# Performance work log

Measured on AMD Instinct MI355X. Metric: run time of the kernel, lower is better.

## Reference

```python
import jax, jax.numpy as jnp
import numpy as np

N, E, H, NH, RBF = 20000, 200000, 128, 8, 64
HD = H // NH
CUT_HI = 5.0


def _ln(t, s, b, eps=1e-6):
    mu = t.mean(-1, keepdims=True)
    var = ((t - mu) ** 2).mean(-1, keepdims=True)
    return (t - mu) * jax.lax.rsqrt(var + eps) * s + b


def _cutoff(w):
    # cosine cutoff, cutoff_lower = 0
    return 0.5 * (jnp.cos(w * (jnp.pi / CUT_HI)) + 1.0) * (w < CUT_HI)


def _xavier(k, fi, fo):
    lim = float(np.sqrt(6.0 / (fi + fo)))
    return jax.random.uniform(k, (fi, fo), minval=-lim, maxval=lim, dtype=jnp.float32)


def setup_inputs() -> dict:
    key = jax.random.key(0)
    ks = jax.random.split(key, 16)
    return {
        "x": jax.random.normal(ks[0], (N, H), jnp.float32),
        "vec": jax.random.normal(ks[1], (N, 3, H), jnp.float32),
        "edge_weight": jax.random.uniform(ks[2], (E, 1), jnp.float32) * 6.0,
        "edge_attr": jax.random.uniform(ks[3], (E, RBF), jnp.float32),
        "edge_vec": jax.random.normal(ks[4], (E, 3), jnp.float32),
        "senders": jax.random.randint(ks[5], (E,), 0, N, jnp.int32),
        "receivers": jax.random.randint(ks[6], (E,), 0, N, jnp.int32),
        "ln_s": jnp.ones((H,), jnp.float32), "ln_b": jnp.zeros((H,), jnp.float32),
        "Wq": _xavier(ks[7], H, H), "bq": jnp.zeros((H,), jnp.float32),
        "Wk": _xavier(ks[8], H, H), "bk": jnp.zeros((H,), jnp.float32),
        "Wv": _xavier(ks[9], H, 3 * H), "bv": jnp.zeros((3 * H,), jnp.float32),
        "Wvec": _xavier(ks[10], H, 3 * H),
        "Wdk": _xavier(ks[11], RBF, H), "bdk": jnp.zeros((H,), jnp.float32),
        "Wdv": _xavier(ks[12], RBF, 3 * H), "bdv": jnp.zeros((3 * H,), jnp.float32),
        "Wo": _xavier(ks[13], H, 3 * H), "bo": jnp.zeros((3 * H,), jnp.float32),
        "qln_s": jnp.ones((HD,), jnp.float32), "qln_b": jnp.zeros((HD,), jnp.float32),
        "kln_s": jnp.ones((HD,), jnp.float32), "kln_b": jnp.zeros((HD,), jnp.float32),
    }


def reference(x, vec, edge_weight, edge_attr, edge_vec, senders, receivers,
              ln_s, ln_b, Wq, bq, Wk, bk, Wv, bv, Wvec, Wdk, bdk, Wdv, bdv,
              Wo, bo, qln_s, qln_b, kln_s, kln_b):
    act = jax.nn.silu
    n = x.shape[0]
    xn = _ln(x, ln_s, ln_b)                                    # [N,H]
    q = _ln((xn @ Wq + bq).reshape(n, NH, HD), qln_s, qln_b)   # [N,h,d]
    k = _ln((xn @ Wk + bk).reshape(n, NH, HD), kln_s, kln_b)   # [N,h,d]
    v = (xn @ Wv + bv).reshape(n, NH, 3 * HD)                  # [N,h,3d]
    vp = vec @ Wvec                                            # [N,3,3H]
    vec1, vec2, vec3 = jnp.split(vp, 3, axis=-1)               # [N,3,H] each
    vec_dot = (vec1 * vec2).sum(axis=1)                        # [N,H]
    vec_h = vec.reshape(n, 3, NH, HD)                          # [N,3,h,d]
    dk = act(edge_attr @ Wdk + bdk).reshape(-1, NH, HD)        # [E,h,d]
    dv = act(edge_attr @ Wdv + bdv).reshape(-1, NH, 3 * HD)    # [E,h,3d]
    # message
    attn = (q[receivers] * k[senders] * dk).sum(axis=-1)       # [E,h]
    attn = act(attn) * _cutoff(edge_weight)                    # [E,h]
    v_j = v[senders] * dv                                      # [E,h,3d]
    xm, m1, m2 = jnp.split(v_j, 3, axis=2)                     # [E,h,d]
    xm = xm * attn[:, :, None]                                 # [E,h,d]
    vec_m = vec_h[senders] * m1[:, None] + m2[:, None] * edge_vec[:, :, None, None]  # [E,3,h,d]
    # aggregate
    x_agg = jax.ops.segment_sum(xm, receivers, num_segments=n).reshape(n, H)
    vec_agg = jax.ops.segment_sum(vec_m, receivers, num_segments=n).reshape(n, 3, H)
    o1, o2, o3 = jnp.split(x_agg @ Wo + bo, 3, axis=1)         # [N,H] each
    dvec = vec3 * o1[:, None] + vec_agg                        # [N,3,H]
    dx = vec_dot * o2 + o3                                     # [N,H]
    return (dx, dvec)
```

## Files before the change

kernel.cpp:

```cpp
#include <hip/hip_runtime.h>
#include <stdint.h>

#define NN 20000
#define NE 200000

typedef __attribute__((ext_vector_type(8))) short bf16x8;
typedef __attribute__((ext_vector_type(4))) float f32x4;

__device__ __forceinline__ float bf2f(uint32_t u) {
  union { uint32_t i; float f; } v; v.i = u << 16; return v.f;
}
__device__ __forceinline__ uint16_t f2bf(float f) {
  union { float f; uint32_t i; } v; v.f = f;
  return (uint16_t)((v.i + 0x7fffu + ((v.i >> 16) & 1u)) >> 16);
}
__device__ __forceinline__ float siluf(float x) { return x / (1.f + __expf(-x)); }


__global__ void k_transpose_cast(const float* __restrict__ src, uint16_t* __restrict__ dst,
                                 int K, int C) {
  int idx = blockIdx.x * 256 + threadIdx.x;
  if (idx >= K * C) return;
  int c = idx / K, k = idx - c * K;
  dst[idx] = f2bf(src[(size_t)k * C + c]);
}

__global__ void k_bias_concat(const float* __restrict__ bq, const float* __restrict__ bk,
                              const float* __restrict__ bv, const float* __restrict__ bdk,
                              const float* __restrict__ bdv, float* __restrict__ Bqkv,
                              float* __restrict__ Bdkv) {
  int t = blockIdx.x * 256 + threadIdx.x;
  if (t < 640) Bqkv[t] = (t < 128) ? bq[t] : ((t < 256) ? bk[t - 128] : bv[t - 256]);
  if (t < 512) Bdkv[t] = (t < 128) ? bdk[t] : bdv[t - 128];
}

__global__ void k_ln_cast(const float* __restrict__ x, const float* __restrict__ s,
                          const float* __restrict__ b, uint16_t* __restrict__ out) {
  int gt = blockIdx.x * 256 + threadIdx.x;
  int node = gt >> 6, lane = gt & 63;
  if (node >= NN) return;
  const float* row = x + (size_t)node * 128;
  float2 v = *(const float2*)&row[lane * 2];
  float sum = v.x + v.y, sq = v.x * v.x + v.y * v.y;
  #pragma unroll
  for (int off = 32; off; off >>= 1) { sum += __shfl_xor(sum, off); sq += __shfl_xor(sq, off); }
  float mu = sum * (1.f / 128.f);
  float var = sq * (1.f / 128.f) - mu * mu;
  float rs = rsqrtf(var + 1e-6f);
  float o0 = (v.x - mu) * rs * s[lane * 2] + b[lane * 2];
  float o1 = (v.y - mu) * rs * s[lane * 2 + 1] + b[lane * 2 + 1];
  ((uint32_t*)out)[(size_t)node * 64 + lane] = (uint32_t)f2bf(o0) | ((uint32_t)f2bf(o1) << 16);
}

__global__ void k_cast_bf16(const float* __restrict__ src, uint16_t* __restrict__ dst, int npairs) {
  int i = blockIdx.x * 256 + threadIdx.x;
  if (i >= npairs) return;
  float2 v = ((const float2*)src)[i];
  ((uint32_t*)dst)[i] = (uint32_t)f2bf(v.x) | ((uint32_t)f2bf(v.y) << 16);
}

__global__ void k_hist(const int* __restrict__ rcv, int* __restrict__ deg) {
  int e = blockIdx.x * 256 + threadIdx.x;
  if (e < NE) atomicAdd(&deg[rcv[e]], 1);
}

__global__ void k_scan1(const int* __restrict__ deg, int* __restrict__ bsum) {
  __shared__ int ws[4];
  int i = blockIdx.x * 256 + threadIdx.x;
  int x = (i < NN) ? deg[i] : 0;
  #pragma unroll
  for (int d = 32; d; d >>= 1) x += __shfl_xor(x, d);
  if ((threadIdx.x & 63) == 0) ws[threadIdx.x >> 6] = x;
  __syncthreads();
  if (threadIdx.x == 0) bsum[blockIdx.x] = ws[0] + ws[1] + ws[2] + ws[3];
}

__global__ void k_scan2(int* __restrict__ bsum, int nb, int* __restrict__ off) {
  int lane = threadIdx.x;
  int carry = 0;
  for (int base = 0; base < nb; base += 64) {
    int i = base + lane;
    int x = (i < nb) ? bsum[i] : 0;
    int v = x;
    #pragma unroll
    for (int d = 1; d < 64; d <<= 1) { int y = __shfl_up(v, d); if (lane >= d) v += y; }
    if (i < nb) bsum[i] = carry + v - x;
    carry += __shfl(v, 63);
  }
  if (lane == 0) off[NN] = carry;
}

__global__ void k_scan3(const int* __restrict__ deg, const int* __restrict__ bsum,
                        int* __restrict__ off, int* __restrict__ cur) {
  __shared__ int ws[4];
  int t = threadIdx.x, lane = t & 63, w = t >> 6;
  int i = blockIdx.x * 256 + t;
  int x = (i < NN) ? deg[i] : 0;
  int v = x;
  #pragma unroll
  for (int d = 1; d < 64; d <<= 1) { int y = __shfl_up(v, d); if (lane >= d) v += y; }
  if (lane == 63) ws[w] = v;
  __syncthreads();
  int wadd = 0;
  for (int j = 0; j < w; j++) wadd += ws[j];
  int excl = bsum[blockIdx.x] + wadd + v - x;
  if (i < NN) { off[i] = excl; cur[i] = excl; }
}

__global__ void k_scatter(const int* __restrict__ rcv, int* __restrict__ cur,
                          int* __restrict__ perm) {
  int e = blockIdx.x * 256 + threadIdx.x;
  if (e >= NE) return;
  int pos = atomicAdd(&cur[rcv[e]], 1);
  perm[pos] = e;
}

__global__ void k_permute(const float* __restrict__ ea, const int* __restrict__ perm,
                          const int* __restrict__ snd, const float* __restrict__ ew,
                          const float* __restrict__ evec, uint16_t* __restrict__ ea_perm,
                          int* __restrict__ sndp, float4* __restrict__ edata) {
  int idx = blockIdx.x * 256 + threadIdx.x;
  if (idx >= NE * 16) return;
  int i = idx >> 4, j = idx & 15;
  int e = perm[i];
  float4 v = *(const float4*)&ea[(size_t)e * 64 + j * 4];
  uint2 o;
  o.x = (uint32_t)f2bf(v.x) | ((uint32_t)f2bf(v.y) << 16);
  o.y = (uint32_t)f2bf(v.z) | ((uint32_t)f2bf(v.w) << 16);
  *(uint2*)&ea_perm[(size_t)i * 64 + j * 4] = o;
  if (j == 0) {
    sndp[i] = snd[e];
    edata[i] = make_float4(evec[e * 3], evec[e * 3 + 1], evec[e * 3 + 2], ew[e]);
  }
}

template <int KTOT, bool OUT_BF16, bool SILU>
__global__ __launch_bounds__(256) void k_gemm(const uint16_t* __restrict__ A,
                                              const uint16_t* __restrict__ BT,
                                              const float* __restrict__ bias,
                                              void* __restrict__ Cout, int M, int Fo) {
  __shared__ __align__(16) uint16_t As[128 * 72];
  __shared__ __align__(16) uint16_t Bs[128 * 72];
  int t = threadIdx.x;
  int l = t & 63;
  int row0 = blockIdx.y * 128, col0 = blockIdx.x * 128;
  int wm = ((t >> 6) >> 1) * 64, wn = ((t >> 6) & 1) * 64;
  f32x4 acc[4][4] = {};
  for (int kt = 0; kt < KTOT; kt += 64) {
    __syncthreads();
    #pragma unroll
    for (int i = 0; i < 4; i++) {
      int c = i * 256 + t;
      int row = c >> 3, ko = (c & 7) * 8;
      uint4 av = make_uint4(0u, 0u, 0u, 0u);
      int gr = row0 + row;
      if (gr < M) av = *(const uint4*)&A[(size_t)gr * KTOT + kt + ko];
      *(uint4*)&As[row * 72 + ko] = av;
      uint4 bw = *(const uint4*)&BT[(size_t)(col0 + row) * KTOT + kt + ko];
      *(uint4*)&Bs[row * 72 + ko] = bw;
    }
    __syncthreads();
    #pragma unroll
    for (int kk = 0; kk < 64; kk += 32) {
      bf16x8 af[4], bfr[4];
      #pragma unroll
      for (int mf = 0; mf < 4; mf++)
        af[mf] = *(const bf16x8*)&As[(wm + mf * 16 + (l & 15)) * 72 + (l >> 4) * 8 + kk];
      #pragma unroll
      for (int nf = 0; nf < 4; nf++)
        bfr[nf] = *(const bf16x8*)&Bs[(wn + nf * 16 + (l & 15)) * 72 + (l >> 4) * 8 + kk];
      #pragma unroll
      for (int mf = 0; mf < 4; mf++)
        #pragma unroll
        for (int nf = 0; nf < 4; nf++)
          acc[mf][nf] = __builtin_amdgcn_mfma_f32_16x16x32_bf16(af[mf], bfr[nf], acc[mf][nf], 0, 0, 0);
    }
  }
  float* Cf = (float*)Cout;
  uint16_t* Cb = (uint16_t*)Cout;
  #pragma unroll
  for (int mf = 0; mf < 4; mf++) {
    #pragma unroll
    for (int r = 0; r < 4; r++) {
      int grow = row0 + wm + mf * 16 + (l >> 4) * 4 + r;
      if (grow >= M) continue;
      #pragma unroll
      for (int nf = 0; nf < 4; nf++) {
        int gcol = col0 + wn + nf * 16 + (l & 15);
        float v = acc[mf][nf][r];
        if (bias) v += bias[gcol];
        if (SILU) v = siluf(v);
        if (OUT_BF16) Cb[(size_t)grow * Fo + gcol] = f2bf(v);
        else          Cf[(size_t)grow * Fo + gcol] = v;
      }
    }
  }
}

__global__ __launch_bounds__(256) void k_gemm_dkv(const uint16_t* __restrict__ Aperm,
                                                  const int* __restrict__ pbeg,
                                                  const int* __restrict__ pend,
                                                  const uint16_t* __restrict__ BT,
                                                  const float* __restrict__ bias,
                                                  uint16_t* __restrict__ Cout, int Mcap) {
  int e0 = pbeg[0];
  int M = pend[0] - e0;
  if (M > Mcap) M = Mcap;
  int row0 = blockIdx.y * 128, col0 = blockIdx.x * 128;
  if (row0 >= M) return;
  const uint16_t* A = Aperm + (size_t)e0 * 64;
  __shared__ __align__(16) uint16_t As[128 * 72];
  __shared__ __align__(16) uint16_t Bs[128 * 72];
  int t = threadIdx.x;
  int l = t & 63;
  int wm = ((t >> 6) >> 1) * 64, wn = ((t >> 6) & 1) * 64;
  f32x4 acc[4][4] = {};
  {
    #pragma unroll
    for (int i = 0; i < 4; i++) {
      int c = i * 256 + t;
      int row = c >> 3, ko = (c & 7) * 8;
      uint4 av = make_uint4(0u, 0u, 0u, 0u);
      if (row0 + row < M) av = *(const uint4*)&A[(size_t)(row0 + row) * 64 + ko];
      *(uint4*)&As[row * 72 + ko] = av;
      uint4 bw = *(const uint4*)&BT[(size_t)(col0 + row) * 64 + ko];
      *(uint4*)&Bs[row * 72 + ko] = bw;
    }
    __syncthreads();
    #pragma unroll
    for (int kk = 0; kk < 64; kk += 32) {
      bf16x8 af[4], bfr[4];
      #pragma unroll
      for (int mf = 0; mf < 4; mf++)
        af[mf] = *(const bf16x8*)&As[(wm + mf * 16 + (l & 15)) * 72 + (l >> 4) * 8 + kk];
      #pragma unroll
      for (int nf = 0; nf < 4; nf++)
        bfr[nf] = *(const bf16x8*)&Bs[(wn + nf * 16 + (l & 15)) * 72 + (l >> 4) * 8 + kk];
      #pragma unroll
      for (int mf = 0; mf < 4; mf++)
        #pragma unroll
        for (int nf = 0; nf < 4; nf++)
          acc[mf][nf] = __builtin_amdgcn_mfma_f32_16x16x32_bf16(af[mf], bfr[nf], acc[mf][nf], 0, 0, 0);
    }
  }
  #pragma unroll
  for (int mf = 0; mf < 4; mf++) {
    #pragma unroll
    for (int r = 0; r < 4; r++) {
      int grow = row0 + wm + mf * 16 + (l >> 4) * 4 + r;
      if (grow >= M) continue;
      #pragma unroll
      for (int nf = 0; nf < 4; nf++) {
        int gcol = col0 + wn + nf * 16 + (l & 15);
        float v = siluf(acc[mf][nf][r] + bias[gcol]);
        Cout[(size_t)grow * 512 + gcol] = f2bf(v);
      }
    }
  }
}

__global__ void k_headln(const uint16_t* __restrict__ qkv, const float* __restrict__ qs,
                         const float* __restrict__ qb, const float* __restrict__ ks,
                         const float* __restrict__ kb, uint16_t* __restrict__ out) {
  int idx = blockIdx.x * 256 + threadIdx.x;
  if (idx >= NN * 16) return;
  int n = idx >> 4, ph = idx & 15, part = ph >> 3, h = ph & 7;
  const uint16_t* src = qkv + (size_t)n * 640 + part * 128 + h * 16;
  float v[16], sum = 0.f;
  #pragma unroll
  for (int i = 0; i < 16; i++) { v[i] = bf2f(src[i]); sum += v[i]; }
  float mu = sum * (1.f / 16.f), var = 0.f;
  #pragma unroll
  for (int i = 0; i < 16; i++) { float d = v[i] - mu; var += d * d; }
  float rs = rsqrtf(var * (1.f / 16.f) + 1e-6f);
  const float* sc = part ? ks : qs;
  const float* bb = part ? kb : qb;
  uint16_t* dst = out + (size_t)n * 256 + part * 128 + h * 16;
  #pragma unroll
  for (int i = 0; i < 16; i++) dst[i] = f2bf((v[i] - mu) * rs * sc[i] + bb[i]);
}

__global__ __launch_bounds__(128) void k_agg(
    const uint16_t* __restrict__ dkdv, const int* __restrict__ off,
    const int* __restrict__ sndp, const float4* __restrict__ edata,
    const uint16_t* __restrict__ qk_b, const uint16_t* __restrict__ qkv_b,
    const uint16_t* __restrict__ vec_b, float* __restrict__ xagg,
    float* __restrict__ vecagg, int n0, int n1, int Mcap) {
  int n = n0 + blockIdx.x;
  if (n >= n1) return;
  int hd = threadIdx.x, h = hd >> 4, d = hd & 15;
  int i0 = off[n], i1 = off[n + 1];
  int ebase = off[n0];
  float q = bf2f(qk_b[(size_t)n * 256 + hd]);
  int vb = h * 48 + d;
  float ax = 0.f, a0 = 0.f, a1 = 0.f, a2 = 0.f;
  for (int i = i0; i < i1; i++) {
    int li = i - ebase;
    if (li >= Mcap) break;
    int s = sndp[i];
    float4 ed = edata[i];
    const uint16_t* row = dkdv + (size_t)li * 512;
    float dk = bf2f(row[hd]);
    float kv = bf2f(qk_b[(size_t)s * 256 + 128 + hd]);
    float t = q * kv * dk;
    t += __shfl_xor(t, 1); t += __shfl_xor(t, 2);
    t += __shfl_xor(t, 4); t += __shfl_xor(t, 8);
    float w = ed.w;
    float cut = (w < 5.f) ? 0.5f * (__cosf(w * 0.628318530717958648f) + 1.f) : 0.f;
    float a = (t / (1.f + __expf(-t))) * cut;
    float dv0 = bf2f(row[128 + vb]), dv1 = bf2f(row[144 + vb]), dv2 = bf2f(row[160 + vb]);
    const uint16_t* vsp = qkv_b + (size_t)s * 640 + 256 + vb;
    float m1 = bf2f(vsp[16]) * dv1;
    float m2 = bf2f(vsp[32]) * dv2;
    ax += bf2f(vsp[0]) * dv0 * a;
    const uint16_t* vv = vec_b + (size_t)s * 384;
    a0 += bf2f(vv[hd]) * m1 + m2 * ed.x;
    a1 += bf2f(vv[128 + hd]) * m1 + m2 * ed.y;
    a2 += bf2f(vv[256 + hd]) * m1 + m2 * ed.z;
  }
  xagg[(size_t)n * 128 + hd] = ax;
  vecagg[((size_t)n * 3 + 0) * 128 + hd] = a0;
  vecagg[((size_t)n * 3 + 1) * 128 + hd] = a1;
  vecagg[((size_t)n * 3 + 2) * 128 + hd] = a2;
}

__global__ void k_final(const float* __restrict__ o, const uint16_t* __restrict__ vp,
                        float* __restrict__ dx, float* __restrict__ dvec) {
  int idx = blockIdx.x * 256 + threadIdx.x;
  if (idx >= NN * 128) return;
  int n = idx >> 7, j = idx & 127;
  const float* op = o + (size_t)n * 384;
  float o1 = op[j], o2 = op[128 + j], o3 = op[256 + j];
  const uint16_t* vpn = vp + (size_t)n * 3 * 384;
  float vd = 0.f;
  #pragma unroll
  for (int c = 0; c < 3; c++)
    vd += bf2f(vpn[c * 384 + j]) * bf2f(vpn[c * 384 + 128 + j]);
  dx[idx] = vd * o2 + o3;
  #pragma unroll
  for (int c = 0; c < 3; c++) {
    size_t vi = ((size_t)n * 3 + c) * 128 + j;
    dvec[vi] = bf2f(vpn[c * 384 + 256 + j]) * o1 + dvec[vi];
  }
}

static inline int cdiv_i(long long a, long long b) { return (int)((a + b - 1) / b); }

extern "C" void kernel_launch(void* const* d_in, const int* in_sizes, int n_in,
                              void* d_out, int out_size, void* d_ws, size_t ws_size,
                              hipStream_t stream) {
  const float* x    = (const float*)d_in[0];
  const float* vec  = (const float*)d_in[1];
  const float* ew   = (const float*)d_in[2];
  const float* ea   = (const float*)d_in[3];
  const float* evec = (const float*)d_in[4];
  const int*   snd  = (const int*)d_in[5];
  const int*   rcv  = (const int*)d_in[6];
  const float* ln_s = (const float*)d_in[7];
  const float* ln_b = (const float*)d_in[8];
  const float* Wq = (const float*)d_in[9];   const float* bq = (const float*)d_in[10];
  const float* Wk = (const float*)d_in[11];  const float* bk = (const float*)d_in[12];
  const float* Wv = (const float*)d_in[13];  const float* bv = (const float*)d_in[14];
  const float* Wvec = (const float*)d_in[15];
  const float* Wdk = (const float*)d_in[16]; const float* bdk = (const float*)d_in[17];
  const float* Wdv = (const float*)d_in[18]; const float* bdv = (const float*)d_in[19];
  const float* Wo = (const float*)d_in[20];  const float* bo = (const float*)d_in[21];
  const float* qln_s = (const float*)d_in[22]; const float* qln_b = (const float*)d_in[23];
  const float* kln_s = (const float*)d_in[24]; const float* kln_b = (const float*)d_in[25];
  (void)in_sizes; (void)n_in; (void)out_size;

  uint8_t* p = (uint8_t*)d_ws;
  auto alloc = [&](size_t bytes) -> uint8_t* {
    uint8_t* r = p; p += (bytes + 255) & ~(size_t)255; return r;
  };
  uint16_t* WTqkv = (uint16_t*)alloc(640 * 128 * 2);
  float*    Bqkv  = (float*)alloc(640 * 4);
  uint16_t* WTvec = (uint16_t*)alloc(384 * 128 * 2);
  uint16_t* WTdkv = (uint16_t*)alloc(512 * 64 * 2);
  float*    Bdkv  = (float*)alloc(512 * 4);
  uint16_t* WTo   = (uint16_t*)alloc(384 * 128 * 2);
  int*      deg   = (int*)alloc(NN * 4);
  int*      off   = (int*)alloc((NN + 1) * 4);
  int*      cur   = (int*)alloc(NN * 4);
  int*      bsum  = (int*)alloc(256 * 4);
  int*      perm  = (int*)alloc((size_t)NE * 4);
  int*      sndp  = (int*)alloc((size_t)NE * 4);
  float4*   edata = (float4*)alloc((size_t)NE * 16);
  uint16_t* xn_b  = (uint16_t*)alloc((size_t)NN * 128 * 2);
  uint16_t* qkv_b = (uint16_t*)alloc((size_t)NN * 640 * 2);
  uint16_t* qk_b  = (uint16_t*)alloc((size_t)NN * 256 * 2);
  uint16_t* vec_b = (uint16_t*)alloc((size_t)NN * 3 * 128 * 2);
  uint16_t* vp    = (uint16_t*)alloc((size_t)NN * 3 * 384 * 2);
  uint16_t* ea_perm = (uint16_t*)alloc((size_t)NE * 64 * 2);
  float*    o      = (float*)alloc((size_t)NN * 384 * 4);
  uint16_t* xagg_b = (uint16_t*)alloc((size_t)NN * 128 * 2);
  size_t fixed = (size_t)(p - (uint8_t*)d_ws);

  int nchunk = 1;
  long long CHmax = NE;
  for (nchunk = 1; nchunk <= 64; nchunk++) {
    long long base = (NE + nchunk - 1) / nchunk;
    CHmax = (nchunk == 1) ? (long long)NE : base + base / 4;
    if (fixed + (size_t)CHmax * 1024 + 4096 <= ws_size) break;
  }
  uint16_t* dkdv = (uint16_t*)alloc((size_t)CHmax * 1024);
  int NB = cdiv_i(NN, nchunk);

  float* xagg   = (float*)d_out;
  float* vecagg = (float*)d_out + (size_t)NN * 128;

  k_transpose_cast<<<cdiv_i(128 * 128, 256), 256, 0, stream>>>(Wq, WTqkv, 128, 128);
  k_transpose_cast<<<cdiv_i(128 * 128, 256), 256, 0, stream>>>(Wk, WTqkv + 128 * 128, 128, 128);
  k_transpose_cast<<<cdiv_i(384 * 128, 256), 256, 0, stream>>>(Wv, WTqkv + 256 * 128, 128, 384);
  k_transpose_cast<<<cdiv_i(384 * 128, 256), 256, 0, stream>>>(Wvec, WTvec, 128, 384);
  k_transpose_cast<<<cdiv_i(128 * 64, 256), 256, 0, stream>>>(Wdk, WTdkv, 64, 128);
  k_transpose_cast<<<cdiv_i(384 * 64, 256), 256, 0, stream>>>(Wdv, WTdkv + 128 * 64, 64, 384);
  k_transpose_cast<<<cdiv_i(384 * 128, 256), 256, 0, stream>>>(Wo, WTo, 128, 384);
  k_bias_concat<<<3, 256, 0, stream>>>(bq, bk, bv, bdk, bdv, Bqkv, Bdkv);

  int NSB = cdiv_i(NN, 256);
  hipMemsetAsync(deg, 0, NN * 4, stream);
  k_hist<<<cdiv_i(NE, 256), 256, 0, stream>>>(rcv, deg);
  k_scan1<<<NSB, 256, 0, stream>>>(deg, bsum);
  k_scan2<<<1, 64, 0, stream>>>(bsum, NSB, off);
  k_scan3<<<NSB, 256, 0, stream>>>(deg, bsum, off, cur);
  k_scatter<<<cdiv_i(NE, 256), 256, 0, stream>>>(rcv, cur, perm);
  k_permute<<<cdiv_i((long long)NE * 16, 256), 256, 0, stream>>>(ea, perm, snd, ew, evec,
                                                                 ea_perm, sndp, edata);

  k_ln_cast<<<cdiv_i((long long)NN * 64, 256), 256, 0, stream>>>(x, ln_s, ln_b, xn_b);
  k_cast_bf16<<<cdiv_i((long long)NN * 3 * 64, 256), 256, 0, stream>>>(vec, vec_b, NN * 3 * 64);

  { dim3 g(640 / 128, cdiv_i(NN, 128));
    k_gemm<128, true, false><<<g, 256, 0, stream>>>(xn_b, WTqkv, Bqkv, qkv_b, NN, 640); }
  k_headln<<<cdiv_i((long long)NN * 16, 256), 256, 0, stream>>>(qkv_b, qln_s, qln_b, kln_s, kln_b, qk_b);

  { dim3 g(384 / 128, cdiv_i((long long)NN * 3, 128));
    k_gemm<128, true, false><<<g, 256, 0, stream>>>(vec_b, WTvec, nullptr, vp, NN * 3, 384); }

  for (int c = 0; c < nchunk; c++) {
    int nlo = c * NB, nhi = (c + 1) * NB; if (nhi > NN) nhi = NN;
    if (nlo >= nhi) break;
    dim3 g(512 / 128, cdiv_i(CHmax, 128));
    k_gemm_dkv<<<g, 256, 0, stream>>>(ea_perm, &off[nlo], &off[nhi], WTdkv, Bdkv,
                                      dkdv, (int)CHmax);
    k_agg<<<nhi - nlo, 128, 0, stream>>>(dkdv, off, sndp, edata, qk_b, qkv_b,
                                         vec_b, xagg, vecagg, nlo, nhi, (int)CHmax);
  }

  k_cast_bf16<<<cdiv_i((long long)NN * 64, 256), 256, 0, stream>>>(xagg, xagg_b, NN * 64);
  { dim3 g(384 / 128, cdiv_i(NN, 128));
    k_gemm<128, false, false><<<g, 256, 0, stream>>>(xagg_b, WTo, bo, o, NN, 384); }

  k_final<<<cdiv_i((long long)NN * 128, 256), 256, 0, stream>>>(o, vp, xagg, vecagg);
}
```

Measured before the change: 412.3 us.

## Fuse edge-filter GEMM into per-wave edge aggregation with segmented reduction

The separate edge-attribute permute/cast, chunked dk/dv GEMM writing a bf16 intermediate, and per-node aggregation kernel are replaced by one fused kernel. Each wave handles 16 receiver-sorted edges: it loads edge_attr rows through perm, converts them to bf16 in registers, runs MFMAs against the filter weights, applies silu and the message math in registers, then does a segmented reduction over receivers, storing directly when a node's segment lies entirely inside the wave and using atomics otherwise. This removes the dkdv round-trip through memory and the chunking loop, at the cost of a zero-fill of the output, atomics on boundary nodes, high register pressure (32 accumulator fragments) and weight fragments read straight from global memory per wave.

```diff
diff --git a/kernel.cpp b/kernel.cpp
--- a/kernel.cpp
+++ b/kernel.cpp
@@ -13,6 +13,9 @@
 __device__ __forceinline__ uint16_t f2bf(float f) {
   union { float f; uint32_t i; } v; v.f = f;
   return (uint16_t)((v.i + 0x7fffu + ((v.i >> 16) & 1u)) >> 16);
+}
+__device__ __forceinline__ uint32_t pk2(float lo, float hi) {
+  return (uint32_t)f2bf(lo) | ((uint32_t)f2bf(hi) << 16);
 }
 __device__ __forceinline__ float siluf(float x) { return x / (1.f + __expf(-x)); }
 
@@ -49,14 +52,14 @@
   float rs = rsqrtf(var + 1e-6f);
   float o0 = (v.x - mu) * rs * s[lane * 2] + b[lane * 2];
   float o1 = (v.y - mu) * rs * s[lane * 2 + 1] + b[lane * 2 + 1];
-  ((uint32_t*)out)[(size_t)node * 64 + lane] = (uint32_t)f2bf(o0) | ((uint32_t)f2bf(o1) << 16);
+  ((uint32_t*)out)[(size_t)node * 64 + lane] = pk2(o0, o1);
 }
 
 __global__ void k_cast_bf16(const float* __restrict__ src, uint16_t* __restrict__ dst, int npairs) {
   int i = blockIdx.x * 256 + threadIdx.x;
   if (i >= npairs) return;
   float2 v = ((const float2*)src)[i];
-  ((uint32_t*)dst)[i] = (uint32_t)f2bf(v.x) | ((uint32_t)f2bf(v.y) << 16);
+  ((uint32_t*)dst)[i] = pk2(v.x, v.y);
 }
 
 __global__ void k_hist(const int* __restrict__ rcv, int* __restrict__ deg) {
@@ -115,23 +118,16 @@
   perm[pos] = e;
 }
 
-__global__ void k_permute(const float* __restrict__ ea, const int* __restrict__ perm,
-                          const int* __restrict__ snd, const float* __restrict__ ew,
-                          const float* __restrict__ evec, uint16_t* __restrict__ ea_perm,
-                          int* __restrict__ sndp, float4* __restrict__ edata) {
-  int idx = blockIdx.x * 256 + threadIdx.x;
-  if (idx >= NE * 16) return;
-  int i = idx >> 4, j = idx & 15;
+__global__ void k_permute(const int* __restrict__ perm, const int* __restrict__ snd,
+                          const int* __restrict__ rcv, const float* __restrict__ ew,
+                          const float* __restrict__ evec, int* __restrict__ sndp,
+                          int* __restrict__ rcvp, float4* __restrict__ edata) {
+  int i = blockIdx.x * 256 + threadIdx.x;
+  if (i >= NE) return;
   int e = perm[i];
-  float4 v = *(const float4*)&ea[(size_t)e * 64 + j * 4];
-  uint2 o;
-  o.x = (uint32_t)f2bf(v.x) | ((uint32_t)f2bf(v.y) << 16);
-  o.y = (uint32_t)f2bf(v.z) | ((uint32_t)f2bf(v.w) << 16);
-  *(uint2*)&ea_perm[(size_t)i * 64 + j * 4] = o;
-  if (j == 0) {
-    sndp[i] = snd[e];
-    edata[i] = make_float4(evec[e * 3], evec[e * 3 + 1], evec[e * 3 + 2], ew[e]);
-  }
+  sndp[i] = snd[e];
+  rcvp[i] = rcv[e];
+  edata[i] = make_float4(evec[e * 3], evec[e * 3 + 1], evec[e * 3 + 2], ew[e]);
 }
 
 template <int KTOT, bool OUT_BF16, bool SILU>
@@ -197,68 +193,6 @@
   }
 }
 
-__global__ __launch_bounds__(256) void k_gemm_dkv(const uint16_t* __restrict__ Aperm,
-                                                  const int* __restrict__ pbeg,
-                                                  const int* __restrict__ pend,
-                                                  const uint16_t* __restrict__ BT,
-                                                  const float* __restrict__ bias,
-                                                  uint16_t* __restrict__ Cout, int Mcap) {
-  int e0 = pbeg[0];
-  int M = pend[0] - e0;
-  if (M > Mcap) M = Mcap;
-  int row0 = blockIdx.y * 128, col0 = blockIdx.x * 128;
-  if (row0 >= M) return;
-  const uint16_t* A = Aperm + (size_t)e0 * 64;
-  __shared__ __align__(16) uint16_t As[128 * 72];
-  __shared__ __align__(16) uint16_t Bs[128 * 72];
-  int t = threadIdx.x;
-  int l = t & 63;
-  int wm = ((t >> 6) >> 1) * 64, wn = ((t >> 6) & 1) * 64;
-  f32x4 acc[4][4] = {};
-  {
-    #pragma unroll
-    for (int i = 0; i < 4; i++) {
-      int c = i * 256 + t;
-      int row = c >> 3, ko = (c & 7) * 8;
-      uint4 av = make_uint4(0u, 0u, 0u, 0u);
-      if (row0 + row < M) av = *(const uint4*)&A[(size_t)(row0 + row) * 64 + ko];
-      *(uint4*)&As[row * 72 + ko] = av;
-      uint4 bw = *(const uint4*)&BT[(size_t)(col0 + row) * 64 + ko];
-      *(uint4*)&Bs[row * 72 + ko] = bw;
-    }
-    __syncthreads();
-    #pragma unroll
-    for (int kk = 0; kk < 64; kk += 32) {
-      bf16x8 af[4], bfr[4];
-      #pragma unroll
-      for (int mf = 0; mf < 4; mf++)
-        af[mf] = *(const bf16x8*)&As[(wm + mf * 16 + (l & 15)) * 72 + (l >> 4) * 8 + kk];
-      #pragma unroll
-      for (int nf = 0; nf < 4; nf++)
-        bfr[nf] = *(const bf16x8*)&Bs[(wn + nf * 16 + (l & 15)) * 72 + (l >> 4) * 8 + kk];
-      #pragma unroll
-      for (int mf = 0; mf < 4; mf++)
-        #pragma unroll
-        for (int nf = 0; nf < 4; nf++)
-          acc[mf][nf] = __builtin_amdgcn_mfma_f32_16x16x32_bf16(af[mf], bfr[nf], acc[mf][nf], 0, 0, 0);
-    }
-  }
-  #pragma unroll
-  for (int mf = 0; mf < 4; mf++) {
-    #pragma unroll
-    for (int r = 0; r < 4; r++) {
-      int grow = row0 + wm + mf * 16 + (l >> 4) * 4 + r;
-      if (grow >= M) continue;
-      #pragma unroll
-      for (int nf = 0; nf < 4; nf++) {
-        int gcol = col0 + wn + nf * 16 + (l & 15);
-        float v = siluf(acc[mf][nf][r] + bias[gcol]);
-        Cout[(size_t)grow * 512 + gcol] = f2bf(v);
-      }
-    }
-  }
-}
-
 __global__ void k_headln(const uint16_t* __restrict__ qkv, const float* __restrict__ qs,
                          const float* __restrict__ qb, const float* __restrict__ ks,
                          const float* __restrict__ kb, uint16_t* __restrict__ out) {
@@ -271,7 +205,7 @@
   for (int i = 0; i < 16; i++) { v[i] = bf2f(src[i]); sum += v[i]; }
   float mu = sum * (1.f / 16.f), var = 0.f;
   #pragma unroll
-  for (int i = 0; i < 16; i++) { float d = v[i] - mu; var += d * d; }
+  for (int i = 0; i < 16; i++) { float dd = v[i] - mu; var += dd * dd; }
   float rs = rsqrtf(var * (1.f / 16.f) + 1e-6f);
   const float* sc = part ? ks : qs;
   const float* bb = part ? kb : qb;
@@ -280,48 +214,112 @@
   for (int i = 0; i < 16; i++) dst[i] = f2bf((v[i] - mu) * rs * sc[i] + bb[i]);
 }
 
-__global__ __launch_bounds__(128) void k_agg(
-    const uint16_t* __restrict__ dkdv, const int* __restrict__ off,
-    const int* __restrict__ sndp, const float4* __restrict__ edata,
+__global__ __launch_bounds__(256) void k_edge_fused(
+    const float* __restrict__ ea, const int* __restrict__ perm,
+    const int* __restrict__ sndp, const int* __restrict__ rcvp,
+    const int* __restrict__ off, const float4* __restrict__ edata,
+    const uint16_t* __restrict__ WTdkv, const float* __restrict__ Bdkv,
     const uint16_t* __restrict__ qk_b, const uint16_t* __restrict__ qkv_b,
     const uint16_t* __restrict__ vec_b, float* __restrict__ xagg,
-    float* __restrict__ vecagg, int n0, int n1, int Mcap) {
-  int n = n0 + blockIdx.x;
-  if (n >= n1) return;
-  int hd = threadIdx.x, h = hd >> 4, d = hd & 15;
-  int i0 = off[n], i1 = off[n + 1];
-  int ebase = off[n0];
-  float q = bf2f(qk_b[(size_t)n * 256 + hd]);
-  int vb = h * 48 + d;
-  float ax = 0.f, a0 = 0.f, a1 = 0.f, a2 = 0.f;
-  for (int i = i0; i < i1; i++) {
-    int li = i - ebase;
-    if (li >= Mcap) break;
-    int s = sndp[i];
-    float4 ed = edata[i];
-    const uint16_t* row = dkdv + (size_t)li * 512;
-    float dk = bf2f(row[hd]);
-    float kv = bf2f(qk_b[(size_t)s * 256 + 128 + hd]);
-    float t = q * kv * dk;
-    t += __shfl_xor(t, 1); t += __shfl_xor(t, 2);
-    t += __shfl_xor(t, 4); t += __shfl_xor(t, 8);
-    float w = ed.w;
-    float cut = (w < 5.f) ? 0.5f * (__cosf(w * 0.628318530717958648f) + 1.f) : 0.f;
-    float a = (t / (1.f + __expf(-t))) * cut;
-    float dv0 = bf2f(row[128 + vb]), dv1 = bf2f(row[144 + vb]), dv2 = bf2f(row[160 + vb]);
-    const uint16_t* vsp = qkv_b + (size_t)s * 640 + 256 + vb;
-    float m1 = bf2f(vsp[16]) * dv1;
-    float m2 = bf2f(vsp[32]) * dv2;
-    ax += bf2f(vsp[0]) * dv0 * a;
-    const uint16_t* vv = vec_b + (size_t)s * 384;
-    a0 += bf2f(vv[hd]) * m1 + m2 * ed.x;
-    a1 += bf2f(vv[128 + hd]) * m1 + m2 * ed.y;
-    a2 += bf2f(vv[256 + hd]) * m1 + m2 * ed.z;
-  }
-  xagg[(size_t)n * 128 + hd] = ax;
-  vecagg[((size_t)n * 3 + 0) * 128 + hd] = a0;
-  vecagg[((size_t)n * 3 + 1) * 128 + hd] = a1;
-  vecagg[((size_t)n * 3 + 2) * 128 + hd] = a2;
+    float* __restrict__ vecagg) {
+  int wid = blockIdx.x * 4 + (threadIdx.x >> 6);
+  int w0 = wid * 16;
+  if (w0 >= NE) return;
+  int l = threadIdx.x & 63, d = l & 15, g = l >> 4;
+
+  f32x4 acc[32] = {};
+  int erow = perm[w0 + d];
+  const float* arow = ea + (size_t)erow * 64 + g * 8;
+  #pragma unroll
+  for (int kk = 0; kk < 2; kk++) {
+    float4 fa = *(const float4*)&arow[kk * 32];
+    float4 fb = *(const float4*)&arow[kk * 32 + 4];
+    union { bf16x8 v; uint32_t u[4]; } apk;
+    apk.u[0] = pk2(fa.x, fa.y); apk.u[1] = pk2(fa.z, fa.w);
+    apk.u[2] = pk2(fb.x, fb.y); apk.u[3] = pk2(fb.z, fb.w);
+    #pragma unroll
+    for (int nf = 0; nf < 32; nf++) {
+      bf16x8 bv = *(const bf16x8*)&WTdkv[(size_t)(nf * 16 + d) * 64 + kk * 32 + g * 8];
+      acc[nf] = __builtin_amdgcn_mfma_f32_16x16x32_bf16(apk.v, bv, acc[nf], 0, 0, 0);
+    }
+  }
+
+  int rcv_[4], snd_[4];
+  float cut_[4], ev0[4], ev1[4], ev2[4];
+  #pragma unroll
+  for (int r = 0; r < 4; r++) {
+    int e = w0 + 4 * g + r;
+    rcv_[r] = rcvp[e]; snd_[r] = sndp[e];
+    float4 ed = edata[e];
+    ev0[r] = ed.x; ev1[r] = ed.y; ev2[r] = ed.z;
+    cut_[r] = (ed.w < 5.f) ? 0.5f * (__cosf(ed.w * 0.628318530717958648f) + 1.f) : 0.f;
+  }
+
+  #pragma unroll
+  for (int h = 0; h < 8; h++) {
+    float bdk_ = Bdkv[h * 16 + d];
+    float b0 = Bdkv[128 + h * 48 + d];
+    float b1 = Bdkv[128 + h * 48 + 16 + d];
+    float b2 = Bdkv[128 + h * 48 + 32 + d];
+    float att[4];
+    #pragma unroll
+    for (int r = 0; r < 4; r++) {
+      float dk = siluf(acc[h][r] + bdk_);
+      float qv = bf2f(qk_b[(size_t)rcv_[r] * 256 + h * 16 + d]);
+      float kv = bf2f(qk_b[(size_t)snd_[r] * 256 + 128 + h * 16 + d]);
+      float t = qv * kv * dk;
+      t += __shfl_xor(t, 1); t += __shfl_xor(t, 2);
+      t += __shfl_xor(t, 4); t += __shfl_xor(t, 8);
+      att[r] = siluf(t) * cut_[r];
+    }
+    #pragma unroll
+    for (int r = 0; r < 4; r++) {
+      float dv0 = siluf(acc[8 + 3 * h][r] + b0);
+      float dv1 = siluf(acc[9 + 3 * h][r] + b1);
+      float dv2 = siluf(acc[10 + 3 * h][r] + b2);
+      const uint16_t* vrow = qkv_b + (size_t)snd_[r] * 640 + 256 + h * 48;
+      float xm = bf2f(vrow[d]) * dv0 * att[r];
+      float m1 = bf2f(vrow[16 + d]) * dv1;
+      float m2 = bf2f(vrow[32 + d]) * dv2;
+      const uint16_t* vecrow = vec_b + (size_t)snd_[r] * 384 + h * 16 + d;
+      acc[h][r] = xm;
+      acc[8 + 3 * h][r]  = bf2f(vecrow[0])   * m1 + m2 * ev0[r];
+      acc[9 + 3 * h][r]  = bf2f(vecrow[128]) * m1 + m2 * ev1[r];
+      acc[10 + 3 * h][r] = bf2f(vecrow[256]) * m1 + m2 * ev2[r];
+    }
+  }
+
+  int w1 = w0 + 16;
+  int i = w0;
+  while (i < w1) {
+    int n = rcvp[i];
+    int a = off[n], b = off[n + 1];
+    int lo = i - w0;
+    int hi = (b < w1 ? b : w1) - w0;
+    bool whole = (a >= w0) && (b <= w1);
+    #pragma unroll
+    for (int f = 0; f < 32; f++) {
+      float s = 0.f;
+      #pragma unroll
+      for (int r = 0; r < 4; r++) {
+        int rr = 4 * g + r;
+        s += (rr >= lo && rr < hi) ? acc[f][r] : 0.f;
+      }
+      s += __shfl_xor(s, 16);
+      s += __shfl_xor(s, 32);
+      if (g == (f & 3)) {
+        float* dst;
+        if (f < 8) {
+          dst = &xagg[(size_t)n * 128 + f * 16 + d];
+        } else {
+          int hh = (f - 8) / 3, cc = (f - 8) % 3;
+          dst = &vecagg[((size_t)n * 3 + cc) * 128 + hh * 16 + d];
+        }
+        if (whole) *dst = s; else atomicAdd(dst, s);
+      }
+    }
+    i = (b > i) ? b : (i + 1);
+  }
 }
 
 __global__ void k_final(const float* __restrict__ o, const uint16_t* __restrict__ vp,
@@ -367,7 +365,7 @@
   const float* Wo = (const float*)d_in[20];  const float* bo = (const float*)d_in[21];
   const float* qln_s = (const float*)d_in[22]; const float* qln_b = (const float*)d_in[23];
   const float* kln_s = (const float*)d_in[24]; const float* kln_b = (const float*)d_in[25];
-  (void)in_sizes; (void)n_in; (void)out_size;
+  (void)in_sizes; (void)n_in; (void)out_size; (void)ws_size;
 
   uint8_t* p = (uint8_t*)d_ws;
   auto alloc = [&](size_t bytes) -> uint8_t* {
@@ -385,29 +383,20 @@
   int*      bsum  = (int*)alloc(256 * 4);
   int*      perm  = (int*)alloc((size_t)NE * 4);
   int*      sndp  = (int*)alloc((size_t)NE * 4);
+  int*      rcvp  = (int*)alloc((size_t)NE * 4);
   float4*   edata = (float4*)alloc((size_t)NE * 16);
   uint16_t* xn_b  = (uint16_t*)alloc((size_t)NN * 128 * 2);
   uint16_t* qkv_b = (uint16_t*)alloc((size_t)NN * 640 * 2);
   uint16_t* qk_b  = (uint16_t*)alloc((size_t)NN * 256 * 2);
   uint16_t* vec_b = (uint16_t*)alloc((size_t)NN * 3 * 128 * 2);
   uint16_t* vp    = (uint16_t*)alloc((size_t)NN * 3 * 384 * 2);
-  uint16_t* ea_perm = (uint16_t*)alloc((size_t)NE * 64 * 2);
-  float*    o      = (float*)alloc((size_t)NN * 384 * 4);
+  float*    o     = (float*)alloc((size_t)NN * 384 * 4);
   uint16_t* xagg_b = (uint16_t*)alloc((size_t)NN * 128 * 2);
-  size_t fixed = (size_t)(p - (uint8_t*)d_ws);
-
-  int nchunk = 1;
-  long long CHmax = NE;
-  for (nchunk = 1; nchunk <= 64; nchunk++) {
-    long long base = (NE + nchunk - 1) / nchunk;
-    CHmax = (nchunk == 1) ? (long long)NE : base + base / 4;
-    if (fixed + (size_t)CHmax * 1024 + 4096 <= ws_size) break;
-  }
-  uint16_t* dkdv = (uint16_t*)alloc((size_t)CHmax * 1024);
-  int NB = cdiv_i(NN, nchunk);
 
   float* xagg   = (float*)d_out;
   float* vecagg = (float*)d_out + (size_t)NN * 128;
+
+  hipMemsetAsync(d_out, 0, (size_t)out_size * 4, stream);
 
   k_transpose_cast<<<cdiv_i(128 * 128, 256), 256, 0, stream>>>(Wq, WTqkv, 128, 128);
   k_transpose_cast<<<cdiv_i(128 * 128, 256), 256, 0, stream>>>(Wk, WTqkv + 128 * 128, 128, 128);
@@ -425,8 +414,7 @@
   k_scan2<<<1, 64, 0, stream>>>(bsum, NSB, off);
   k_scan3<<<NSB, 256, 0, stream>>>(deg, bsum, off, cur);
   k_scatter<<<cdiv_i(NE, 256), 256, 0, stream>>>(rcv, cur, perm);
-  k_permute<<<cdiv_i((long long)NE * 16, 256), 256, 0, stream>>>(ea, perm, snd, ew, evec,
-                                                                 ea_perm, sndp, edata);
+  k_permute<<<cdiv_i(NE, 256), 256, 0, stream>>>(perm, snd, rcv, ew, evec, sndp, rcvp, edata);
 
   k_ln_cast<<<cdiv_i((long long)NN * 64, 256), 256, 0, stream>>>(x, ln_s, ln_b, xn_b);
   k_cast_bf16<<<cdiv_i((long long)NN * 3 * 64, 256), 256, 0, stream>>>(vec, vec_b, NN * 3 * 64);
@@ -438,15 +426,8 @@
   { dim3 g(384 / 128, cdiv_i((long long)NN * 3, 128));
     k_gemm<128, true, false><<<g, 256, 0, stream>>>(vec_b, WTvec, nullptr, vp, NN * 3, 384); }
 
-  for (int c = 0; c < nchunk; c++) {
-    int nlo = c * NB, nhi = (c + 1) * NB; if (nhi > NN) nhi = NN;
-    if (nlo >= nhi) break;
-    dim3 g(512 / 128, cdiv_i(CHmax, 128));
-    k_gemm_dkv<<<g, 256, 0, stream>>>(ea_perm, &off[nlo], &off[nhi], WTdkv, Bdkv,
-                                      dkdv, (int)CHmax);
-    k_agg<<<nhi - nlo, 128, 0, stream>>>(dkdv, off, sndp, edata, qk_b, qkv_b,
-                                         vec_b, xagg, vecagg, nlo, nhi, (int)CHmax);
-  }
+  k_edge_fused<<<NE / 64, 256, 0, stream>>>(ea, perm, sndp, rcvp, off, edata, WTdkv,
+                                            Bdkv, qk_b, qkv_b, vec_b, xagg, vecagg);
 
   k_cast_bf16<<<cdiv_i((long long)NN * 64, 256), 256, 0, stream>>>(xagg, xagg_b, NN * 64);
   { dim3 g(384 / 128, cdiv_i(NN, 128));
```

New measurement: 985.7 us. 2.39x slower.

## Fuse attention score computation into edge GEMM epilogue, drop dk intermediate

Applied to the files above, without the earlier changes.

The edge GEMM epilogue for the dk column block now gathers q[receiver] and k[sender], reduces the per-head dot product, applies silu and the cutoff, and writes a compact per-edge, per-head attention buffer instead of a bf16 dk tile. The dv part is written to a narrower buffer, and the cosine cutoff is precomputed once in the permute kernel. The aggregation kernel then reads only attention scalars and dv, which cuts per-edge traffic in k_agg. The cost is random q/k gathers inside the GEMM epilogue and an extra receiver-permutation array.

```diff
diff --git a/kernel.cpp b/kernel.cpp
--- a/kernel.cpp
+++ b/kernel.cpp
@@ -13,6 +13,9 @@
 __device__ __forceinline__ uint16_t f2bf(float f) {
   union { float f; uint32_t i; } v; v.f = f;
   return (uint16_t)((v.i + 0x7fffu + ((v.i >> 16) & 1u)) >> 16);
+}
+__device__ __forceinline__ uint32_t pk2(float lo, float hi) {
+  return (uint32_t)f2bf(lo) | ((uint32_t)f2bf(hi) << 16);
 }
 __device__ __forceinline__ float siluf(float x) { return x / (1.f + __expf(-x)); }
 
@@ -49,14 +52,14 @@
   float rs = rsqrtf(var + 1e-6f);
   float o0 = (v.x - mu) * rs * s[lane * 2] + b[lane * 2];
   float o1 = (v.y - mu) * rs * s[lane * 2 + 1] + b[lane * 2 + 1];
-  ((uint32_t*)out)[(size_t)node * 64 + lane] = (uint32_t)f2bf(o0) | ((uint32_t)f2bf(o1) << 16);
+  ((uint32_t*)out)[(size_t)node * 64 + lane] = pk2(o0, o1);
 }
 
 __global__ void k_cast_bf16(const float* __restrict__ src, uint16_t* __restrict__ dst, int npairs) {
   int i = blockIdx.x * 256 + threadIdx.x;
   if (i >= npairs) return;
   float2 v = ((const float2*)src)[i];
-  ((uint32_t*)dst)[i] = (uint32_t)f2bf(v.x) | ((uint32_t)f2bf(v.y) << 16);
+  ((uint32_t*)dst)[i] = pk2(v.x, v.y);
 }
 
 __global__ void k_hist(const int* __restrict__ rcv, int* __restrict__ deg) {
@@ -116,21 +119,25 @@
 }
 
 __global__ void k_permute(const float* __restrict__ ea, const int* __restrict__ perm,
-                          const int* __restrict__ snd, const float* __restrict__ ew,
-                          const float* __restrict__ evec, uint16_t* __restrict__ ea_perm,
-                          int* __restrict__ sndp, float4* __restrict__ edata) {
+                          const int* __restrict__ snd, const int* __restrict__ rcv,
+                          const float* __restrict__ ew, const float* __restrict__ evec,
+                          uint16_t* __restrict__ ea_perm, int* __restrict__ sndp,
+                          int* __restrict__ rcvp, float4* __restrict__ edata) {
   int idx = blockIdx.x * 256 + threadIdx.x;
   if (idx >= NE * 16) return;
   int i = idx >> 4, j = idx & 15;
   int e = perm[i];
   float4 v = *(const float4*)&ea[(size_t)e * 64 + j * 4];
   uint2 o;
-  o.x = (uint32_t)f2bf(v.x) | ((uint32_t)f2bf(v.y) << 16);
-  o.y = (uint32_t)f2bf(v.z) | ((uint32_t)f2bf(v.w) << 16);
+  o.x = pk2(v.x, v.y);
+  o.y = pk2(v.z, v.w);
   *(uint2*)&ea_perm[(size_t)i * 64 + j * 4] = o;
   if (j == 0) {
     sndp[i] = snd[e];
-    edata[i] = make_float4(evec[e * 3], evec[e * 3 + 1], evec[e * 3 + 2], ew[e]);
+    rcvp[i] = rcv[e];
+    float w = ew[e];
+    float cut = (w < 5.f) ? 0.5f * (__cosf(w * 0.628318530717958648f) + 1.f) : 0.f;
+    edata[i] = make_float4(evec[e * 3], evec[e * 3 + 1], evec[e * 3 + 2], cut);
   }
 }
 
@@ -197,12 +204,13 @@
   }
 }
 
-__global__ __launch_bounds__(256) void k_gemm_dkv(const uint16_t* __restrict__ Aperm,
-                                                  const int* __restrict__ pbeg,
-                                                  const int* __restrict__ pend,
-                                                  const uint16_t* __restrict__ BT,
-                                                  const float* __restrict__ bias,
-                                                  uint16_t* __restrict__ Cout, int Mcap) {
+__global__ __launch_bounds__(256) void k_edge_gemm(
+    const uint16_t* __restrict__ Aperm, const int* __restrict__ pbeg,
+    const int* __restrict__ pend, const uint16_t* __restrict__ BT,
+    const float* __restrict__ Bdkv, const int* __restrict__ sndp,
+    const int* __restrict__ rcvp, const float4* __restrict__ edata,
+    const uint16_t* __restrict__ qk_b, float* __restrict__ attnb,
+    uint16_t* __restrict__ dvb, int Mcap) {
   int e0 = pbeg[0];
   int M = pend[0] - e0;
   if (M > Mcap) M = Mcap;
@@ -243,17 +251,44 @@
           acc[mf][nf] = __builtin_amdgcn_mfma_f32_16x16x32_bf16(af[mf], bfr[nf], acc[mf][nf], 0, 0, 0);
     }
   }
-  #pragma unroll
-  for (int mf = 0; mf < 4; mf++) {
-    #pragma unroll
-    for (int r = 0; r < 4; r++) {
-      int grow = row0 + wm + mf * 16 + (l >> 4) * 4 + r;
-      if (grow >= M) continue;
-      #pragma unroll
-      for (int nf = 0; nf < 4; nf++) {
-        int gcol = col0 + wn + nf * 16 + (l & 15);
-        float v = siluf(acc[mf][nf][r] + bias[gcol]);
-        Cout[(size_t)grow * 512 + gcol] = f2bf(v);
+  int d = l & 15;
+  if (col0 == 0) {
+    #pragma unroll
+    for (int mf = 0; mf < 4; mf++) {
+      #pragma unroll
+      for (int r = 0; r < 4; r++) {
+        int lrow = row0 + wm + mf * 16 + (l >> 4) * 4 + r;
+        if (lrow >= M) continue;
+        int ge = e0 + lrow;
+        int rn = rcvp[ge], sn = sndp[ge];
+        float cut = edata[ge].w;
+        #pragma unroll
+        for (int nf = 0; nf < 4; nf++) {
+          int h = (wn >> 4) + nf;
+          float dk = siluf(acc[mf][nf][r] + Bdkv[h * 16 + d]);
+          float qv = bf2f(qk_b[(size_t)rn * 256 + h * 16 + d]);
+          float kv = bf2f(qk_b[(size_t)sn * 256 + 128 + h * 16 + d]);
+          float tt = qv * kv * dk;
+          tt += __shfl_xor(tt, 1); tt += __shfl_xor(tt, 2);
+          tt += __shfl_xor(tt, 4); tt += __shfl_xor(tt, 8);
+          if (d == 0) attnb[(size_t)ge * 8 + h] = siluf(tt) * cut;
+        }
+      }
+    }
+  } else {
+    int cb = col0 - 128;
+    #pragma unroll
+    for (int mf = 0; mf < 4; mf++) {
+      #pragma unroll
+      for (int r = 0; r < 4; r++) {
+        int grow = row0 + wm + mf * 16 + (l >> 4) * 4 + r;
+        if (grow >= M) continue;
+        #pragma unroll
+        for (int nf = 0; nf < 4; nf++) {
+          int gcol = wn + nf * 16 + d;
+          float v = siluf(acc[mf][nf][r] + Bdkv[col0 + gcol]);
+          dvb[(size_t)grow * 384 + cb + gcol] = f2bf(v);
+        }
       }
     }
   }
@@ -271,7 +306,7 @@
   for (int i = 0; i < 16; i++) { v[i] = bf2f(src[i]); sum += v[i]; }
   float mu = sum * (1.f / 16.f), var = 0.f;
   #pragma unroll
-  for (int i = 0; i < 16; i++) { float d = v[i] - mu; var += d * d; }
+  for (int i = 0; i < 16; i++) { float dd = v[i] - mu; var += dd * dd; }
   float rs = rsqrtf(var * (1.f / 16.f) + 1e-6f);
   const float* sc = part ? ks : qs;
   const float* bb = part ? kb : qb;
@@ -281,9 +316,9 @@
 }
 
 __global__ __launch_bounds__(128) void k_agg(
-    const uint16_t* __restrict__ dkdv, const int* __restrict__ off,
-    const int* __restrict__ sndp, const float4* __restrict__ edata,
-    const uint16_t* __restrict__ qk_b, const uint16_t* __restrict__ qkv_b,
+    const uint16_t* __restrict__ dvb, const float* __restrict__ attnb,
+    const int* __restrict__ off, const int* __restrict__ sndp,
+    const float4* __restrict__ edata, const uint16_t* __restrict__ qkv_b,
     const uint16_t* __restrict__ vec_b, float* __restrict__ xagg,
     float* __restrict__ vecagg, int n0, int n1, int Mcap) {
   int n = n0 + blockIdx.x;
@@ -291,28 +326,20 @@
   int hd = threadIdx.x, h = hd >> 4, d = hd & 15;
   int i0 = off[n], i1 = off[n + 1];
   int ebase = off[n0];
-  float q = bf2f(qk_b[(size_t)n * 256 + hd]);
   int vb = h * 48 + d;
   float ax = 0.f, a0 = 0.f, a1 = 0.f, a2 = 0.f;
   for (int i = i0; i < i1; i++) {
     int li = i - ebase;
     if (li >= Mcap) break;
     int s = sndp[i];
-    float4 ed = edata[i];
-    const uint16_t* row = dkdv + (size_t)li * 512;
-    float dk = bf2f(row[hd]);
-    float kv = bf2f(qk_b[(size_t)s * 256 + 128 + hd]);
-    float t = q * kv * dk;
-    t += __shfl_xor(t, 1); t += __shfl_xor(t, 2);
-    t += __shfl_xor(t, 4); t += __shfl_xor(t, 8);
-    float w = ed.w;
-    float cut = (w < 5.f) ? 0.5f * (__cosf(w * 0.628318530717958648f) + 1.f) : 0.f;
-    float a = (t / (1.f + __expf(-t))) * cut;
-    float dv0 = bf2f(row[128 + vb]), dv1 = bf2f(row[144 + vb]), dv2 = bf2f(row[160 + vb]);
+    float a = attnb[(size_t)i * 8 + h];
+    const uint16_t* row = dvb + (size_t)li * 384;
+    float dv0 = bf2f(row[vb]), dv1 = bf2f(row[16 + vb]), dv2 = bf2f(row[32 + vb]);
     const uint16_t* vsp = qkv_b + (size_t)s * 640 + 256 + vb;
     float m1 = bf2f(vsp[16]) * dv1;
     float m2 = bf2f(vsp[32]) * dv2;
     ax += bf2f(vsp[0]) * dv0 * a;
+    float4 ed = edata[i];
     const uint16_t* vv = vec_b + (size_t)s * 384;
     a0 += bf2f(vv[hd]) * m1 + m2 * ed.x;
     a1 += bf2f(vv[128 + hd]) * m1 + m2 * ed.y;
@@ -385,6 +412,7 @@
   int*      bsum  = (int*)alloc(256 * 4);
   int*      perm  = (int*)alloc((size_t)NE * 4);
   int*      sndp  = (int*)alloc((size_t)NE * 4);
+  int*      rcvp  = (int*)alloc((size_t)NE * 4);
   float4*   edata = (float4*)alloc((size_t)NE * 16);
   uint16_t* xn_b  = (uint16_t*)alloc((size_t)NN * 128 * 2);
   uint16_t* qkv_b = (uint16_t*)alloc((size_t)NN * 640 * 2);
@@ -392,6 +420,7 @@
   uint16_t* vec_b = (uint16_t*)alloc((size_t)NN * 3 * 128 * 2);
   uint16_t* vp    = (uint16_t*)alloc((size_t)NN * 3 * 384 * 2);
   uint16_t* ea_perm = (uint16_t*)alloc((size_t)NE * 64 * 2);
+  float*    attnb = (float*)alloc((size_t)NE * 8 * 4);
   float*    o      = (float*)alloc((size_t)NN * 384 * 4);
   uint16_t* xagg_b = (uint16_t*)alloc((size_t)NN * 128 * 2);
   size_t fixed = (size_t)(p - (uint8_t*)d_ws);
@@ -401,9 +430,9 @@
   for (nchunk = 1; nchunk <= 64; nchunk++) {
     long long base = (NE + nchunk - 1) / nchunk;
     CHmax = (nchunk == 1) ? (long long)NE : base + base / 4;
-    if (fixed + (size_t)CHmax * 1024 + 4096 <= ws_size) break;
-  }
-  uint16_t* dkdv = (uint16_t*)alloc((size_t)CHmax * 1024);
+    if (fixed + (size_t)CHmax * 768 + 4096 <= ws_size) break;
+  }
+  uint16_t* dvb = (uint16_t*)alloc((size_t)CHmax * 768);
   int NB = cdiv_i(NN, nchunk);
 
   float* xagg   = (float*)d_out;
@@ -425,8 +454,8 @@
   k_scan2<<<1, 64, 0, stream>>>(bsum, NSB, off);
   k_scan3<<<NSB, 256, 0, stream>>>(deg, bsum, off, cur);
   k_scatter<<<cdiv_i(NE, 256), 256, 0, stream>>>(rcv, cur, perm);
-  k_permute<<<cdiv_i((long long)NE * 16, 256), 256, 0, stream>>>(ea, perm, snd, ew, evec,
-                                                                 ea_perm, sndp, edata);
+  k_permute<<<cdiv_i((long long)NE * 16, 256), 256, 0, stream>>>(ea, perm, snd, rcv, ew, evec,
+                                                                 ea_perm, sndp, rcvp, edata);
 
   k_ln_cast<<<cdiv_i((long long)NN * 64, 256), 256, 0, stream>>>(x, ln_s, ln_b, xn_b);
   k_cast_bf16<<<cdiv_i((long long)NN * 3 * 64, 256), 256, 0, stream>>>(vec, vec_b, NN * 3 * 64);
@@ -441,10 +470,10 @@
   for (int c = 0; c < nchunk; c++) {
     int nlo = c * NB, nhi = (c + 1) * NB; if (nhi > NN) nhi = NN;
     if (nlo >= nhi) break;
-    dim3 g(512 / 128, cdiv_i(CHmax, 128));
-    k_gemm_dkv<<<g, 256, 0, stream>>>(ea_perm, &off[nlo], &off[nhi], WTdkv, Bdkv,
-                                      dkdv, (int)CHmax);
-    k_agg<<<nhi - nlo, 128, 0, stream>>>(dkdv, off, sndp, edata, qk_b, qkv_b,
+    dim3 g(4, cdiv_i(CHmax, 128));
+    k_edge_gemm<<<g, 256, 0, stream>>>(ea_perm, &off[nlo], &off[nhi], WTdkv, Bdkv,
+                                       sndp, rcvp, edata, qk_b, attnb, dvb, (int)CHmax);
+    k_agg<<<nhi - nlo, 128, 0, stream>>>(dvb, attnb, off, sndp, edata, qkv_b,
                                          vec_b, xagg, vecagg, nlo, nhi, (int)CHmax);
   }
 
```

Result: slower. 614.5 us (+49.0%).
